# Kernel tuning notes

Hardware: AMD Instinct MI355X
Metric: run time of the kernel (lower is better)

## Reference

```python
import jax, jax.numpy as jnp
import numpy as np

R = 2          # pool ratio -> context window = R * P
P = 8          # patch_size
STRIDE = 8     # window_stride
NH = 8         # n_heads
EPS = 1e-6


def _partition_nonoverlap(x, ws):
    # (N,C,H,W) -> (N*nH*nW, C, ws, ws), matches F.unfold path with padding 0
    n, c, h, w = x.shape
    x = x.reshape(n, c, h // ws, ws, w // ws, ws)
    x = jnp.transpose(x, (0, 2, 4, 1, 3, 5))
    return x.reshape(-1, c, ws, ws)


def _partition_overlap(x, ws, stride):
    # (N,C,H,W) -> (N*nH*nW, C, ws, ws) with padding (ws-stride)//2, matching F.unfold
    n, c, h, w = x.shape
    pad = (ws - stride) // 2
    xp = jnp.pad(x, ((0, 0), (0, 0), (pad, pad), (pad, pad)))
    ih = (jnp.arange(h // stride) * stride)[:, None] + jnp.arange(ws)[None, :]
    iw = (jnp.arange(w // stride) * stride)[:, None] + jnp.arange(ws)[None, :]
    xw = xp[:, :, ih, :]          # (n, c, nH, ws, Wp)
    xw = xw[:, :, :, :, iw]       # (n, c, nH, ws, nW, ws)
    xw = jnp.transpose(xw, (0, 2, 4, 1, 3, 5))  # (n, nH, nW, c, ws, ws)
    return xw.reshape(-1, c, ws, ws)


def setup_inputs() -> dict:
    key = jax.random.key(0)
    ks = jax.random.split(key, 4)
    C = 512
    x = jax.random.normal(ks[0], (1, C, 128, 128), jnp.float32)
    ln_w = jnp.ones((C,), jnp.float32)
    ln_b = jnp.zeros((C,), jnp.float32)
    mix_w = jax.random.normal(ks[1], (NH, P * P, P * P), jnp.float32) * 0.02
    mix_b = jnp.zeros((NH, P * P), jnp.float32)
    in_w = jax.random.normal(ks[2], (3 * C, C), jnp.float32) * 0.02
    in_b = jnp.zeros((3 * C,), jnp.float32)
    out_w = jax.random.normal(ks[3], (C, C), jnp.float32) * 0.02
    out_b = jnp.zeros((C,), jnp.float32)
    return dict(x=x, ln_w=ln_w, ln_b=ln_b, mix_w=mix_w, mix_b=mix_b,
                in_w=in_w, in_b=in_b, out_w=out_w, out_b=out_b)


def reference(x, ln_w, ln_b, mix_w, mix_b, in_w, in_b, out_w, out_b):
    n, c, h, w = x.shape
    ws = R * P
    L = P * P  # 64 positions per window

    # query windows: non-overlapping 8x8 patches -> (B, L, C)
    q = _partition_nonoverlap(x, P)
    q = q.reshape(-1, c, L).transpose(0, 2, 1)

    # context windows: 16x16 overlapping, avg-pooled r x r -> 8x8 -> (B, L, C)
    ctx = _partition_overlap(x, ws, STRIDE)
    ctx = ctx.reshape(-1, c, P, R, P, R).mean(axis=(3, 5))  # AvgPool2d(r, r)
    ctx = ctx.reshape(-1, c, L).transpose(0, 2, 1)

    # LayerNorm over channel dim (eps 1e-6, biased variance)
    mu = ctx.mean(-1, keepdims=True)
    var = ctx.var(-1, keepdims=True)
    ctx = (ctx - mu) / jnp.sqrt(var + EPS) * ln_w + ln_b

    # PositionMixing: per-head Linear(64,64) over the L axis + residual
    B = ctx.shape[0]
    t = ctx.transpose(0, 2, 1).reshape(B, NH, c // NH, L)  # (B, H, hd, L)
    mixed = jnp.einsum('bhcl,hml->bhcm', t, mix_w) + mix_b[None, :, None, :]
    ctx = (t + mixed).reshape(B, c, L).transpose(0, 2, 1)  # (B, L, C)

    # nn.MultiheadAttention with batch_first=False (torch default):
    # first dim B (windows) is the SEQUENCE, second dim L=64 is the BATCH.
    hd = c // NH
    Wq, Wk, Wv = in_w[:c], in_w[c:2 * c], in_w[2 * c:]
    bq, bk, bv = in_b[:c], in_b[c:2 * c], in_b[2 * c:]
    Q = (jnp.einsum('slc,ec->sle', q, Wq) + bq).reshape(B, L, NH, hd)
    K = (jnp.einsum('slc,ec->sle', ctx, Wk) + bk).reshape(B, L, NH, hd)
    V = (jnp.einsum('slc,ec->sle', ctx, Wv) + bv).reshape(B, L, NH, hd)
    scale = 1.0 / jnp.sqrt(jnp.asarray(hd, x.dtype))
    scores = jnp.einsum('slhd,tlhd->lhst', Q, K) * scale  # (L, H, B, B)
    attn = jax.nn.softmax(scores, axis=-1)
    o = jnp.einsum('lhst,tlhd->slhd', attn, V).reshape(B, L, c)
    o = jnp.einsum('slc,ec->sle', o, out_w) + out_b

    # nlc_to_nchw + window_reverse -> (N, C, H, W)
    o = o.transpose(0, 2, 1).reshape(B, c, P, P)
    o = o.reshape(n, h // P, w // P, c, P, P)
    o = jnp.transpose(o, (0, 3, 1, 4, 2, 5)).reshape(n, c, h, w)
    return o
```

## Files before the change

### kernel.cpp

```cpp
#include <hip/hip_runtime.h>


typedef __bf16 bf16;
typedef __bf16 bf16x2 __attribute__((ext_vector_type(2)));
typedef __bf16 bf16x4 __attribute__((ext_vector_type(4)));
typedef __bf16 bf16x8 __attribute__((ext_vector_type(8)));
typedef float f32x4 __attribute__((ext_vector_type(4)));

#define MFMA(a, b, c) __builtin_amdgcn_mfma_f32_16x16x32_bf16(a, b, c, 0, 0, 0)

__device__ __forceinline__ void gll16(const void* g, void* l) {
  __builtin_amdgcn_global_load_lds((const __attribute__((address_space(1))) void*)g,
                                   (__attribute__((address_space(3))) void*)l, 16, 0, 0);
}

__global__ void k_wconv(const float* __restrict__ in_w, const float* __restrict__ out_w,
                        bf16* __restrict__ wib, bf16* __restrict__ wob) {
  int i = blockIdx.x * blockDim.x + threadIdx.x;
  const int n1 = (1536 * 512) / 4;
  float4 v;
  bf16* dst;
  if (i < n1) { v = ((const float4*)in_w)[i];      dst = wib + (size_t)i * 4; }
  else        { v = ((const float4*)out_w)[i - n1]; dst = wob + (size_t)(i - n1) * 4; }
  dst[0] = (bf16)v.x; dst[1] = (bf16)v.y; dst[2] = (bf16)v.z; dst[3] = (bf16)v.w;
}

__global__ __launch_bounds__(256) void k_pq(const float* __restrict__ x,
                                            float* __restrict__ xp2t,
                                            bf16* __restrict__ qb) {
  __shared__ float xs[2][64][133];
  const int y2 = blockIdx.x, c0 = blockIdx.y * 64, t = threadIdx.x;
  #pragma unroll
  for (int it = 0; it < 16; ++it) {
    int flat = it * 256 + t;
    int ci = flat >> 6, rest = flat & 63;
    int yb = rest >> 5, xq = rest & 31;
    float4 v = *(const float4*)(x + (size_t)(c0 + ci) * 16384 +
                                (size_t)(2 * y2 + yb) * 128 + xq * 4);
    float* d = &xs[yb][ci][xq * 4];
    d[0] = v.x; d[1] = v.y; d[2] = v.z; d[3] = v.w;
  }
  __syncthreads();
  #pragma unroll
  for (int it = 0; it < 16; ++it) {
    int flat = it * 256 + t;
    int x2 = flat >> 6, ci = flat & 63;
    float s = xs[0][ci][2 * x2] + xs[0][ci][2 * x2 + 1] +
              xs[1][ci][2 * x2] + xs[1][ci][2 * x2 + 1];
    xp2t[(size_t)(y2 * 64 + x2) * 512 + c0 + ci] = 0.25f * s;
  }
  #pragma unroll
  for (int yb = 0; yb < 2; ++yb) {
    const int Y = 2 * y2 + yb;
    const int hy = Y >> 3, py = Y & 7;
    #pragma unroll
    for (int it = 0; it < 32; ++it) {
      int flat = it * 256 + t;
      int X = flat >> 6, ci = flat & 63;
      int l = py * 8 + (X & 7), s = hy * 16 + (X >> 3);
      qb[((size_t)l * 256 + s) * 512 + c0 + ci] = (bf16)xs[yb][ci][X];
    }
  }
}

__global__ __launch_bounds__(512) void k_ln(const float* __restrict__ xp2t,
                                            const float* __restrict__ lnw,
                                            const float* __restrict__ lnb,
                                            bf16* __restrict__ T) {
  __shared__ bf16 Tt[512][24];
  const int s = blockIdx.x, qt = blockIdx.y;
  const int wy = s >> 4, wx = s & 15;
  const int t = threadIdx.x, wv = t >> 6, ln = t & 63;

  float wl[8], bl[8];
  #pragma unroll
  for (int k = 0; k < 8; ++k) { wl[k] = lnw[k * 64 + ln]; bl[k] = lnb[k * 64 + ln]; }

  float v[2][8], mu_[2], rs_[2];
  #pragma unroll
  for (int p = 0; p < 2; ++p) {
    const int l = qt * 16 + wv * 2 + p;
    const int py = l >> 3, px = l & 7;
    const int y2 = wy * 4 - 2 + py, x2 = wx * 4 - 2 + px;
    const bool inb = (y2 >= 0) && (y2 < 64) && (x2 >= 0) && (x2 < 64);
    const float* src = xp2t + (size_t)(y2 * 64 + x2) * 512;
    float sum = 0.f, ssq = 0.f;
    #pragma unroll
    for (int k = 0; k < 8; ++k) {
      float xv = 0.f;
      if (inb) xv = src[k * 64 + ln];
      v[p][k] = xv; sum += xv; ssq += xv * xv;
    }
    #pragma unroll
    for (int off = 1; off < 64; off <<= 1) {
      sum += __shfl_xor(sum, off);
      ssq += __shfl_xor(ssq, off);
    }
    float mu = sum * (1.f / 512.f);
    mu_[p] = mu;
    rs_[p] = rsqrtf(ssq * (1.f / 512.f) - mu * mu + 1e-6f);
  }
  #pragma unroll
  for (int k = 0; k < 8; ++k) {
    const int c = k * 64 + ln;
    bf16x2 u;
    u.x = (bf16)((v[0][k] - mu_[0]) * rs_[0] * wl[k] + bl[k]);
    u.y = (bf16)((v[1][k] - mu_[1]) * rs_[1] * wl[k] + bl[k]);
    *(bf16x2*)(&Tt[c][wv * 2]) = u;
  }
  __syncthreads();
  #pragma unroll
  for (int it = 0; it < 2; ++it) {
    int flat = it * 512 + t;
    int c = flat >> 1, ch = flat & 1;
    bf16x8 u = *(const bf16x8*)(&Tt[c][ch * 8]);
    *(bf16x8*)(T + ((size_t)s * 512 + c) * 64 + qt * 16 + ch * 8) = u;
  }
}

__global__ __launch_bounds__(256) void k_mix(const bf16* __restrict__ T,
                                             const float* __restrict__ mix_w,
                                             const float* __restrict__ mix_b,
                                             bf16* __restrict__ ctx) {
  const int t = threadIdx.x, wv = t >> 6, ln = t & 63;
  const int s = blockIdx.x, hg = blockIdx.y;
  const int h = hg * 4 + wv;
  const int q = ln >> 4, r = ln & 15;

  bf16x8 a[4][2];
  #pragma unroll
  for (int m = 0; m < 4; ++m) {
    #pragma unroll
    for (int ks = 0; ks < 2; ++ks) {
      const int rm = m * 16 + r;
      const float* wsrc = mix_w + ((size_t)h * 64 + rm) * 64 + ks * 32 + q * 8;
      bf16x8 pk;
      #pragma unroll
      for (int e = 0; e < 8; ++e) {
        int l = ks * 32 + q * 8 + e;
        float w = wsrc[e] + (rm == l ? 1.f : 0.f);
        pk[e] = (bf16)w;
      }
      a[m][ks] = pk;
    }
  }
  const bf16* Tb = T + ((size_t)s * 512 + h * 64) * 64;
  bf16x8 b[4][2];
  #pragma unroll
  for (int n = 0; n < 4; ++n) {
    #pragma unroll
    for (int ks = 0; ks < 2; ++ks)
      b[n][ks] = *(const bf16x8*)(Tb + (size_t)(n * 16 + r) * 64 + ks * 32 + q * 8);
  }
  f32x4 acc[4][4] = {};
  #pragma unroll
  for (int ks = 0; ks < 2; ++ks) {
    #pragma unroll
    for (int m = 0; m < 4; ++m) {
      #pragma unroll
      for (int n = 0; n < 4; ++n) acc[m][n] = MFMA(a[m][ks], b[n][ks], acc[m][n]);
    }
  }
  #pragma unroll
  for (int m = 0; m < 4; ++m) {
    #pragma unroll
    for (int j = 0; j < 4; ++j) {
      const int rm = m * 16 + q * 4 + j;
      const float bias = mix_b[h * 64 + rm];
      #pragma unroll
      for (int n = 0; n < 4; ++n)
        ctx[((size_t)rm * 256 + s) * 512 + h * 64 + n * 16 + r] =
            (bf16)(acc[m][n][j] + bias);
    }
  }
}

template <int MODE>
__global__ __launch_bounds__(256, 4) void k_gemm(const bf16* __restrict__ A,
                                                 const bf16* __restrict__ B,
                                                 const float* __restrict__ bias,
                                                 bf16* __restrict__ O0,
                                                 bf16* __restrict__ O1) {
  __shared__ bf16 As[8192];
  __shared__ bf16 Bs[8192];
  const int t = threadIdx.x, wv = t >> 6, ln = t & 63;
  const int bm = blockIdx.x, bn = blockIdx.y;
  const int wm = wv >> 1, wn = wv & 1;
  const int q = ln >> 4, r = ln & 15;
  f32x4 acc[4][4] = {};

  const int srow = wv * 8 + (ln >> 3);
  const int swzc = (ln & 7) ^ (ln >> 3);
  const char* ga = (const char*)A + ((size_t)(bm * 128 + srow) * 512) * 2 + swzc * 16;
  const char* gb = (const char*)B + ((size_t)(bn * 128 + srow) * 512) * 2 + swzc * 16;

  for (int k0 = 0; k0 < 512; k0 += 64) {
    #pragma unroll
    for (int i = 0; i < 4; ++i) {
      gll16(ga + (size_t)i * 32 * 1024 + k0 * 2, As + i * 2048 + wv * 512);
      gll16(gb + (size_t)i * 32 * 1024 + k0 * 2, Bs + i * 2048 + wv * 512);
    }
    __syncthreads();
    #pragma unroll
    for (int ks = 0; ks < 2; ++ks) {
      bf16x8 af[4], bfr[4];
      #pragma unroll
      for (int m = 0; m < 4; ++m)
        af[m] = *(const bf16x8*)(As + (wm * 64 + m * 16 + r) * 64 +
                                 (((ks * 4 + q) ^ (r & 7)) * 8));
      #pragma unroll
      for (int n = 0; n < 4; ++n)
        bfr[n] = *(const bf16x8*)(Bs + (wn * 64 + n * 16 + r) * 64 +
                                  (((ks * 4 + q) ^ (r & 7)) * 8));
      #pragma unroll
      for (int m = 0; m < 4; ++m) {
        #pragma unroll
        for (int n = 0; n < 4; ++n) acc[m][n] = MFMA(af[m], bfr[n], acc[m][n]);
      }
    }
    __syncthreads();
  }

  const int r0 = bm * 128 + wm * 64 + q * 4;
  const int c0 = bn * 128 + wn * 64 + r;
  #pragma unroll
  for (int m = 0; m < 4; ++m) {
    const int rg0 = r0 + m * 16;
    #pragma unroll
    for (int n = 0; n < 4; ++n) {
      const int cg = c0 + n * 16;
      const float bv = bias[cg];
      if constexpr (MODE == 2) {
        #pragma unroll
        for (int j = 0; j < 4; ++j)
          O0[(size_t)(rg0 + j) * 512 + cg] = (bf16)(acc[m][n][j] + bv);
      } else if constexpr (MODE == 0) {
        const int li = rg0 >> 8;
        #pragma unroll
        for (int j = 0; j < 4; ++j) {
          int sp = (rg0 + j) & 255;
          O0[(((size_t)li * 8 + (cg >> 6)) * 256 + sp) * 64 + (cg & 63)] =
              (bf16)(acc[m][n][j] + bv);
        }
      } else {
        const int li = rg0 >> 8;
        if (cg < 512) {
          #pragma unroll
          for (int j = 0; j < 4; ++j) {
            int sp = (rg0 + j) & 255;
            O0[(((size_t)li * 8 + (cg >> 6)) * 256 + sp) * 64 + (cg & 63)] =
                (bf16)(acc[m][n][j] + bv);
          }
        } else {
          const int e = cg - 512, hh = e >> 6, d = e & 63;
          const int sp = rg0 & 255;
          bf16x4 pk;
          #pragma unroll
          for (int j = 0; j < 4; ++j) pk[j] = (bf16)(acc[m][n][j] + bv);
          *(bf16x4*)(&O1[(((size_t)li * 8 + hh) * 64 + d) * 256 + sp]) = pk;
        }
      }
    }
  }
}

__global__ __launch_bounds__(256, 4) void k_attn(const bf16* __restrict__ Qa,
                                                 const bf16* __restrict__ Ka,
                                                 const bf16* __restrict__ Vt,
                                                 bf16* __restrict__ Oa) {
  __shared__ bf16 Ks[128 * 64];
  __shared__ bf16 Pw[4][16][132];
  const int t = threadIdx.x, wv = t >> 6, ln = t & 63;
  const int q = ln >> 4, r = ln & 15;
  const int bid = blockIdx.x;
  const int st = (bid >> 3) & 3;
  const int lh = (bid & 7) | ((bid >> 5) << 3);
  const int s0 = st * 64;
  const size_t base = (size_t)lh * (256 * 64);
  const bf16* __restrict__ Qlh = Qa + base;
  const bf16* __restrict__ Klh = Ka + base;
  const bf16* __restrict__ Vlh = Vt + base;
  const float SC = 0.125f * 1.4426950408889634f;

  bf16x8 aq[2];
  #pragma unroll
  for (int ks = 0; ks < 2; ++ks)
    aq[ks] = *(const bf16x8*)(Qlh + (size_t)(s0 + wv * 16 + r) * 64 + ks * 32 + q * 8);

  const int srow = wv * 8 + (ln >> 3);
  const int swzc = (ln & 7) ^ (ln >> 3);
  const char* gk = (const char*)Klh + srow * 128 + swzc * 16;
  #pragma unroll
  for (int i = 0; i < 4; ++i)
    gll16(gk + i * 4096, Ks + i * 2048 + wv * 512);
  __syncthreads();

  f32x4 ao[4] = {};
  float mrun[4], lrun[4];

  #pragma unroll
  for (int h = 0; h < 2; ++h) {
    f32x4 sa[8];
    #pragma unroll
    for (int n = 0; n < 8; ++n) sa[n] = (f32x4){0.f, 0.f, 0.f, 0.f};
    __builtin_amdgcn_s_setprio(1);
    #pragma unroll
    for (int n = 0; n < 8; ++n) {
      const bf16* kr = Ks + (n * 16 + r) * 64;
      bf16x8 b0 = *(const bf16x8*)(kr + ((q ^ (r & 7)) * 8));
      bf16x8 b1 = *(const bf16x8*)(kr + (((4 + q) ^ (r & 7)) * 8));
      sa[n] = MFMA(aq[0], b0, sa[n]);
      sa[n] = MFMA(aq[1], b1, sa[n]);
    }
    __builtin_amdgcn_s_setprio(0);

    if (h == 0) {
      __syncthreads();
      #pragma unroll
      for (int i = 0; i < 4; ++i)
        gll16(gk + 16384 + i * 4096, Ks + i * 2048 + wv * 512);
    }

    #pragma unroll
    for (int j = 0; j < 4; ++j) {
      float mx = sa[0][j];
      #pragma unroll
      for (int n = 1; n < 8; ++n) mx = fmaxf(mx, sa[n][j]);
      #pragma unroll
      for (int off = 1; off < 16; off <<= 1) mx = fmaxf(mx, __shfl_xor(mx, off));
      float mnew = (h == 0) ? mx : fmaxf(mrun[j], mx);
      const float mb = mnew * SC;
      float sm = 0.f;
      #pragma unroll
      for (int n = 0; n < 8; ++n) {
        float p = exp2f(sa[n][j] * SC - mb);
        sa[n][j] = p;
        sm += p;
      }
      #pragma unroll
      for (int off = 1; off < 16; off <<= 1) sm += __shfl_xor(sm, off);
      if (h == 0) {
        mrun[j] = mnew; lrun[j] = sm;
      } else {
        float scale = exp2f(mrun[j] * SC - mb);
        lrun[j] = lrun[j] * scale + sm;
        #pragma unroll
        for (int n = 0; n < 4; ++n) ao[n][j] *= scale;
      }
    }

    #pragma unroll
    for (int n = 0; n < 8; ++n) {
      #pragma unroll
      for (int j = 0; j < 4; ++j)
        Pw[wv][q * 4 + j][n * 16 + r] = (bf16)sa[n][j];
    }
    bf16x8 pa[4];
    #pragma unroll
    for (int ks = 0; ks < 4; ++ks)
      pa[ks] = *(const bf16x8*)(&Pw[wv][r][ks * 32 + q * 8]);

    __builtin_amdgcn_s_setprio(1);
    #pragma unroll
    for (int ks = 0; ks < 4; ++ks) {
      #pragma unroll
      for (int n = 0; n < 4; ++n) {
        bf16x8 vf = *(const bf16x8*)(Vlh + (size_t)(n * 16 + r) * 256 +
                                     h * 128 + ks * 32 + q * 8);
        ao[n] = MFMA(pa[ks], vf, ao[n]);
      }
    }
    __builtin_amdgcn_s_setprio(0);

    if (h == 0) __syncthreads();
  }

  float rr[4];
  #pragma unroll
  for (int j = 0; j < 4; ++j) rr[j] = 1.f / lrun[j];
  bf16* dst = Oa + ((size_t)(lh >> 3) * 256 + s0 + wv * 16 + q * 4) * 512 +
              (lh & 7) * 64 + r;
  #pragma unroll
  for (int j = 0; j < 4; ++j) {
    #pragma unroll
    for (int n = 0; n < 4; ++n)
      dst[(size_t)j * 512 + n * 16] = (bf16)(ao[n][j] * rr[j]);
  }
}

__global__ void k_orelay(const bf16* __restrict__ o_tmp, float* __restrict__ out) {
  __shared__ bf16 buf[64][130];
  const int hy = blockIdx.x, py = blockIdx.y, e0 = blockIdx.z * 64, t = threadIdx.x;
  #pragma unroll
  for (int i = 0; i < 32; ++i) {
    int flat = i * 256 + t;
    int r = flat >> 6, e = flat & 63;
    int px = r >> 4, hx = r & 15;
    buf[e][hx * 8 + px] =
        o_tmp[((size_t)(py * 8 + px) * 256 + hy * 16 + hx) * 512 + e0 + e];
  }
  __syncthreads();
  const int Y = hy * 8 + py;
  #pragma unroll
  for (int i = 0; i < 32; ++i) {
    int flat = i * 256 + t;
    int e = flat >> 7, X = flat & 127;
    out[(size_t)(e0 + e) * 16384 + (size_t)Y * 128 + X] = (float)buf[e][X];
  }
}

extern "C" void kernel_launch(void* const* d_in, const int* in_sizes, int n_in,
                              void* d_out, int out_size, void* d_ws, size_t ws_size,
                              hipStream_t stream) {
  const float* x     = (const float*)d_in[0];
  const float* ln_w  = (const float*)d_in[1];
  const float* ln_b  = (const float*)d_in[2];
  const float* mix_w = (const float*)d_in[3];
  const float* mix_b = (const float*)d_in[4];
  const float* in_w  = (const float*)d_in[5];
  const float* in_b  = (const float*)d_in[6];
  const float* out_w = (const float*)d_in[7];
  const float* out_b = (const float*)d_in[8];
  float* out = (float*)d_out;
  char* ws = (char*)d_ws;

  const size_t MB = 1u << 20;
  float* xp2t = (float*)(ws);
  bf16* qb    = (bf16*)(ws + 8 * MB);
  bf16* Tn    = (bf16*)(ws + 24 * MB);
  bf16* ctxb  = (bf16*)(ws + 40 * MB);
  bf16* Qa    = (bf16*)(ws + 56 * MB);
  bf16* Ka    = (bf16*)(ws);
  bf16* Vt    = (bf16*)(ws + 16 * MB);
  bf16* oatt  = (bf16*)(ws + 32 * MB);
  bf16* otmp  = (bf16*)(ws + 48 * MB);
  bf16* wib   = (bf16*)(ws + 72 * MB);
  bf16* wob   = (bf16*)(ws + 72 * MB + 1572864);

  k_wconv<<<1024, 256, 0, stream>>>(in_w, out_w, wib, wob);
  k_pq<<<dim3(64, 8), 256, 0, stream>>>(x, xp2t, qb);
  k_ln<<<dim3(256, 4), 512, 0, stream>>>(xp2t, ln_w, ln_b, Tn);
  k_mix<<<dim3(256, 2), 256, 0, stream>>>(Tn, mix_w, mix_b, ctxb);
  k_gemm<0><<<dim3(128, 4), 256, 0, stream>>>(qb, wib, in_b, Qa, nullptr);
  k_gemm<1><<<dim3(128, 8), 256, 0, stream>>>(ctxb, wib + 512 * 512, in_b + 512, Ka, Vt);
  k_attn<<<2048, 256, 0, stream>>>(Qa, Ka, Vt, oatt);
  k_gemm<2><<<dim3(128, 4), 256, 0, stream>>>(oatt, wob, out_b, otmp, nullptr);
  k_orelay<<<dim3(16, 8, 8), 256, 0, stream>>>(otmp, out);
}
```

Measured before the change: 148.8 us.

## Transpose QK MFMA so softmax reduces in-lane, prefetch V fragments

Swaps the MFMA operand order in the QK^T product so each lane holds scores for a single query row across keys. The row max and sum become mostly in-register vector reductions needing only two cross-lane shuffles instead of four per row element, and the running max/sum collapse to scalars. V fragments are loaded from global memory before the softmax so their latency overlaps the exp work, and P is written to LDS as packed bf16x4. Occupancy is lowered from 4 to 3 blocks per SIMD to make room for the extra V registers, at the cost of fewer waves for latency hiding.

```diff
diff --git a/kernel.cpp b/kernel.cpp
--- a/kernel.cpp
+++ b/kernel.cpp
@@ -12,6 +12,13 @@
 __device__ __forceinline__ void gll16(const void* g, void* l) {
   __builtin_amdgcn_global_load_lds((const __attribute__((address_space(1))) void*)g,
                                    (__attribute__((address_space(3))) void*)l, 16, 0, 0);
+}
+
+__device__ __forceinline__ f32x4 vmax4(f32x4 a, f32x4 b) {
+  f32x4 c;
+  c[0] = fmaxf(a[0], b[0]); c[1] = fmaxf(a[1], b[1]);
+  c[2] = fmaxf(a[2], b[2]); c[3] = fmaxf(a[3], b[3]);
+  return c;
 }
 
 __global__ void k_wconv(const float* __restrict__ in_w, const float* __restrict__ out_w,
@@ -264,7 +271,7 @@
   }
 }
 
-__global__ __launch_bounds__(256, 4) void k_attn(const bf16* __restrict__ Qa,
+__global__ __launch_bounds__(256, 3) void k_attn(const bf16* __restrict__ Qa,
                                                  const bf16* __restrict__ Ka,
                                                  const bf16* __restrict__ Vt,
                                                  bf16* __restrict__ Oa) {
@@ -296,7 +303,7 @@
   __syncthreads();
 
   f32x4 ao[4] = {};
-  float mrun[4], lrun[4];
+  float mrun = 0.f, lrun = 0.f;
 
   #pragma unroll
   for (int h = 0; h < 2; ++h) {
@@ -307,10 +314,10 @@
     #pragma unroll
     for (int n = 0; n < 8; ++n) {
       const bf16* kr = Ks + (n * 16 + r) * 64;
-      bf16x8 b0 = *(const bf16x8*)(kr + ((q ^ (r & 7)) * 8));
-      bf16x8 b1 = *(const bf16x8*)(kr + (((4 + q) ^ (r & 7)) * 8));
-      sa[n] = MFMA(aq[0], b0, sa[n]);
-      sa[n] = MFMA(aq[1], b1, sa[n]);
+      bf16x8 k0 = *(const bf16x8*)(kr + ((q ^ (r & 7)) * 8));
+      bf16x8 k1 = *(const bf16x8*)(kr + (((4 + q) ^ (r & 7)) * 8));
+      sa[n] = MFMA(k0, aq[0], sa[n]);
+      sa[n] = MFMA(k1, aq[1], sa[n]);
     }
     __builtin_amdgcn_s_setprio(0);
 
@@ -321,39 +328,68 @@
         gll16(gk + 16384 + i * 4096, Ks + i * 2048 + wv * 512);
     }
 
-    #pragma unroll
-    for (int j = 0; j < 4; ++j) {
-      float mx = sa[0][j];
-      #pragma unroll
-      for (int n = 1; n < 8; ++n) mx = fmaxf(mx, sa[n][j]);
-      #pragma unroll
-      for (int off = 1; off < 16; off <<= 1) mx = fmaxf(mx, __shfl_xor(mx, off));
-      float mnew = (h == 0) ? mx : fmaxf(mrun[j], mx);
-      const float mb = mnew * SC;
-      float sm = 0.f;
-      #pragma unroll
-      for (int n = 0; n < 8; ++n) {
-        float p = exp2f(sa[n][j] * SC - mb);
-        sa[n][j] = p;
-        sm += p;
+    bf16x8 bv[4][4];
+    #pragma unroll
+    for (int ks = 0; ks < 4; ++ks) {
+      #pragma unroll
+      for (int n = 0; n < 4; ++n)
+        bv[ks][n] = *(const bf16x8*)(Vlh + (size_t)(n * 16 + r) * 256 +
+                                     h * 128 + ks * 32 + q * 8);
+    }
+
+    f32x4 w4[4];
+    #pragma unroll
+    for (int i = 0; i < 4; ++i) w4[i] = vmax4(sa[i], sa[i + 4]);
+    f32x4 w2a = vmax4(w4[0], w4[2]);
+    f32x4 w2b = vmax4(w4[1], w4[3]);
+    f32x4 w1 = vmax4(w2a, w2b);
+    float mx = fmaxf(fmaxf(w1[0], w1[1]), fmaxf(w1[2], w1[3]));
+    mx = fmaxf(mx, __shfl_xor(mx, 16));
+    mx = fmaxf(mx, __shfl_xor(mx, 32));
+    const float mnew = (h == 0) ? mx : fmaxf(mrun, mx);
+    const float mb = mnew * SC;
+    #pragma unroll
+    for (int n = 0; n < 8; ++n) {
+      #pragma unroll
+      for (int j = 0; j < 4; ++j) sa[n][j] = exp2f(sa[n][j] * SC - mb);
+    }
+    f32x4 u4[4];
+    #pragma unroll
+    for (int i = 0; i < 4; ++i) {
+      u4[i][0] = sa[i][0] + sa[i + 4][0];
+      u4[i][1] = sa[i][1] + sa[i + 4][1];
+      u4[i][2] = sa[i][2] + sa[i + 4][2];
+      u4[i][3] = sa[i][3] + sa[i + 4][3];
+    }
+    f32x4 u2a, u2b;
+    #pragma unroll
+    for (int c = 0; c < 4; ++c) { u2a[c] = u4[0][c] + u4[2][c]; u2b[c] = u4[1][c] + u4[3][c]; }
+    float sum = ((u2a[0] + u2b[0]) + (u2a[1] + u2b[1])) +
+                ((u2a[2] + u2b[2]) + (u2a[3] + u2b[3]));
+    sum += __shfl_xor(sum, 16);
+    sum += __shfl_xor(sum, 32);
+
+    if (h == 0) {
+      mrun = mnew; lrun = sum;
+    } else {
+      const float scale = exp2f(mrun * SC - mb);
+      lrun = lrun * scale + sum;
+      float scj[4];
+      #pragma unroll
+      for (int j = 0; j < 4; ++j) scj[j] = __shfl(scale, q * 4 + j);
+      #pragma unroll
+      for (int n = 0; n < 4; ++n) {
+        #pragma unroll
+        for (int j = 0; j < 4; ++j) ao[n][j] *= scj[j];
       }
-      #pragma unroll
-      for (int off = 1; off < 16; off <<= 1) sm += __shfl_xor(sm, off);
-      if (h == 0) {
-        mrun[j] = mnew; lrun[j] = sm;
-      } else {
-        float scale = exp2f(mrun[j] * SC - mb);
-        lrun[j] = lrun[j] * scale + sm;
-        #pragma unroll
-        for (int n = 0; n < 4; ++n) ao[n][j] *= scale;
-      }
     }
 
     #pragma unroll
     for (int n = 0; n < 8; ++n) {
-      #pragma unroll
-      for (int j = 0; j < 4; ++j)
-        Pw[wv][q * 4 + j][n * 16 + r] = (bf16)sa[n][j];
+      bf16x4 p4;
+      p4[0] = (bf16)sa[n][0]; p4[1] = (bf16)sa[n][1];
+      p4[2] = (bf16)sa[n][2]; p4[3] = (bf16)sa[n][3];
+      *(bf16x4*)(&Pw[wv][r][n * 16 + q * 4]) = p4;
     }
     bf16x8 pa[4];
     #pragma unroll
@@ -364,27 +400,24 @@
     #pragma unroll
     for (int ks = 0; ks < 4; ++ks) {
       #pragma unroll
-      for (int n = 0; n < 4; ++n) {
-        bf16x8 vf = *(const bf16x8*)(Vlh + (size_t)(n * 16 + r) * 256 +
-                                     h * 128 + ks * 32 + q * 8);
-        ao[n] = MFMA(pa[ks], vf, ao[n]);
-      }
+      for (int n = 0; n < 4; ++n) ao[n] = MFMA(pa[ks], bv[ks][n], ao[n]);
     }
     __builtin_amdgcn_s_setprio(0);
 
     if (h == 0) __syncthreads();
   }
 
-  float rr[4];
-  #pragma unroll
-  for (int j = 0; j < 4; ++j) rr[j] = 1.f / lrun[j];
+  const float rr = 1.f / lrun;
+  float rrj[4];
+  #pragma unroll
+  for (int j = 0; j < 4; ++j) rrj[j] = __shfl(rr, q * 4 + j);
   bf16* dst = Oa + ((size_t)(lh >> 3) * 256 + s0 + wv * 16 + q * 4) * 512 +
               (lh & 7) * 64 + r;
   #pragma unroll
   for (int j = 0; j < 4; ++j) {
     #pragma unroll
     for (int n = 0; n < 4; ++n)
-      dst[(size_t)j * 512 + n * 16] = (bf16)(ao[n][j] * rr[j]);
+      dst[(size_t)j * 512 + n * 16] = (bf16)(ao[n][j] * rrj[j]);
   }
 }
 
```

New measurement: 150.1 us. About the same (+0.8%).
